# Optimization experiments

Measured on AMD Instinct MI355X. Metric: run time of the kernel, lower is better.

Reference implementation:

```python
import jax, jax.numpy as jnp
import numpy as np

B, S, D = 16, 2048, 128
NEG = -1e9


def setup_inputs() -> dict:
    key = jax.random.key(0)
    kq, kk, kv = jax.random.split(key, 3)
    queries = jax.random.normal(kq, (B, S, D), dtype=jnp.float32)
    keys = jax.random.normal(kk, (B, S, D), dtype=jnp.float32)
    values = jax.random.normal(kv, (B, S, D), dtype=jnp.float32)
    # causal additive mask: 0 on/below diagonal, -1e9 above
    causal = jnp.triu(jnp.ones((S, S), dtype=jnp.float32), k=1) * NEG
    return {"queries": queries, "keys": keys, "values": values, "mask": causal}


def reference(queries, keys, values, mask):
    d = queries.shape[-1]
    scale = 1.0 / jnp.sqrt(jnp.asarray(d, dtype=queries.dtype))
    # scores: [b, q, k]
    scores = jnp.einsum("bqd,bkd->bqk", queries, keys) * scale
    scores = scores + mask  # broadcast [S,S] over batch
    weights = jax.nn.softmax(scores, axis=-1)
    # dropout p=0.0 in eval mode -> identity
    return jnp.einsum("bqk,bkd->bqd", weights, values)
```

## Files before the change

kernel.cpp:

```cpp
#include <hip/hip_runtime.h>
#include <hip/hip_bf16.h>
#include <cstdint>

#define SS   2048
#define DD   128
#define QBLK 64
#define KBLK 64
#define NTILES (SS / KBLK)
#define TILE_BYTES 16384
#define WS_NEED ((size_t)16 * NTILES * TILE_BYTES * 2)

typedef __attribute__((ext_vector_type(8))) short short8;
typedef __attribute__((ext_vector_type(4))) float f32x4;

__device__ __forceinline__ unsigned short f2bf(float x) {
  return __builtin_bit_cast(unsigned short, (__bf16)x);
}

__device__ __forceinline__ int sigma_col(int a) {
  return (a & 35) | ((a & 12) << 1) | ((a & 16) >> 2);
}

__global__ __launch_bounds__(256) void prepack_kv(
    const float* __restrict__ K, const float* __restrict__ V, char* __restrict__ ws)
{
  __shared__ float vf[64][129];
  const int b = blockIdx.x, t = blockIdx.y;
  const int tid = threadIdx.x;
  const float* Kt = K + ((size_t)b * SS + t * KBLK) * DD;
  const float* Vt = V + ((size_t)b * SS + t * KBLK) * DD;
  char* Kd = ws + ((size_t)(b * NTILES + t)) * TILE_BYTES;
  char* Vd = ws + (size_t)16 * NTILES * TILE_BYTES + ((size_t)(b * NTILES + t)) * TILE_BYTES;

  #pragma unroll
  for (int u = 0; u < 4; ++u) {
    int row = u * 16 + (tid >> 4);
    int col = 8 * (tid & 15);
    const float4* sp = reinterpret_cast<const float4*>(Kt + (size_t)row * DD + col);
    float4 x = sp[0], y = sp[1];
    short8 w;
    w[0] = f2bf(x.x); w[1] = f2bf(x.y); w[2] = f2bf(x.z); w[3] = f2bf(x.w);
    w[4] = f2bf(y.x); w[5] = f2bf(y.y); w[6] = f2bf(y.z); w[7] = f2bf(y.w);
    int off = (row * 256 + col * 2) ^ ((row & 7) << 4);
    *reinterpret_cast<short8*>(Kd + off) = w;
  }
  #pragma unroll
  for (int u = 0; u < 4; ++u) {
    int row = u * 16 + (tid >> 4);
    int col = 8 * (tid & 15);
    const float4* sp = reinterpret_cast<const float4*>(Vt + (size_t)row * DD + col);
    float4 x = sp[0], y = sp[1];
    vf[row][col + 0] = x.x; vf[row][col + 1] = x.y; vf[row][col + 2] = x.z; vf[row][col + 3] = x.w;
    vf[row][col + 4] = y.x; vf[row][col + 5] = y.y; vf[row][col + 6] = y.z; vf[row][col + 7] = y.w;
  }
  __syncthreads();
  #pragma unroll
  for (int q = 0; q < 4; ++q) {
    int idx = q * 256 + tid;
    int d = idx >> 3, y = idx & 7;
    short8 w;
    #pragma unroll
    for (int j = 0; j < 8; ++j) {
      int a = (j & 3) | ((y & 3) << 2) | ((j & 4) << 2) | ((y & 4) << 3);
      w[j] = f2bf(vf[a][d]);
    }
    int off = ((d << 7) + (y << 4)) ^ ((((d >> 3) ^ d) & 7) << 4);
    *reinterpret_cast<short8*>(Vd + off) = w;
  }
}

__device__ __forceinline__ void stage_tile(const char* Ksrc, const char* Vsrc,
                                           char* Kl, char* Vl, int wid, int lane)
{
  #pragma unroll
  for (int i = 0; i < 4; ++i) {
    int off = wid * 4096 + i * 1024;
    __builtin_amdgcn_global_load_lds(
        (const __attribute__((address_space(1))) unsigned int*)(Ksrc + off + lane * 16),
        (__attribute__((address_space(3))) unsigned int*)(Kl + off), 16, 0, 0);
  }
  #pragma unroll
  for (int i = 0; i < 4; ++i) {
    int off = wid * 4096 + i * 1024;
    __builtin_amdgcn_global_load_lds(
        (const __attribute__((address_space(1))) unsigned int*)(Vsrc + off + lane * 16),
        (__attribute__((address_space(3))) unsigned int*)(Vl + off), 16, 0, 0);
  }
}

__global__ __launch_bounds__(256) void sdpa_causal_v2(
    const float* __restrict__ Q, const char* __restrict__ ws, float* __restrict__ O)
{
  __shared__ __align__(16) char smem[2 * 32768];

  const int b = blockIdx.x;
  const int y = blockIdx.y;
  const int qb = (y < 16) ? (31 - y) : (y - 16);
  const int q0 = qb * QBLK;
  const int tid = threadIdx.x;
  const int lane = tid & 63;
  const int wid  = tid >> 6;
  const int l15  = lane & 15;
  const int hi   = lane >> 4;

  const float* Qb = Q + (size_t)b * SS * DD;
  float*       Ob = O + (size_t)b * SS * DD;
  const char*  Kws = ws + ((size_t)b * NTILES) * TILE_BYTES;
  const char*  Vws = ws + (size_t)16 * NTILES * TILE_BYTES + ((size_t)b * NTILES) * TILE_BYTES;

  const float scale = 0.08838834764831845f;

  short8 qf[4];
  {
    const float* qrow = Qb + (size_t)(q0 + wid * 16 + l15) * DD;
    #pragma unroll
    for (int c = 0; c < 4; ++c) {
      const float4* p = reinterpret_cast<const float4*>(qrow + 32 * c + 8 * hi);
      float4 x = p[0], y2 = p[1];
      short8 w;
      w[0] = f2bf(x.x * scale); w[1] = f2bf(x.y * scale);
      w[2] = f2bf(x.z * scale); w[3] = f2bf(x.w * scale);
      w[4] = f2bf(y2.x * scale); w[5] = f2bf(y2.y * scale);
      w[6] = f2bf(y2.z * scale); w[7] = f2bf(y2.w * scale);
      qf[c] = w;
    }
  }

  f32x4 o[8];
  #pragma unroll
  for (int nt = 0; nt < 8; ++nt) o[nt] = (f32x4){0.f, 0.f, 0.f, 0.f};
  float m = -INFINITY;
  float lsum = 0.f;

  const int ntile = qb + 1;
  int cur = 0;

  stage_tile(Kws, Vws, smem, smem + 16384, wid, lane);
  __syncthreads();

  for (int t = 0; t < ntile; ++t) {
    if (t + 1 < ntile) {
      char* nb = smem + (cur ^ 1) * 32768;
      stage_tile(Kws + (size_t)(t + 1) * TILE_BYTES, Vws + (size_t)(t + 1) * TILE_BYTES,
                 nb, nb + 16384, wid, lane);
    }

    const char* Kl = smem + cur * 32768;
    const char* Vl = Kl + 16384;
    const int kv0 = t * KBLK;

    f32x4 sacc[4];
    __builtin_amdgcn_s_setprio(1);
    #pragma unroll
    for (int g = 0; g < 4; ++g) {
      f32x4 acc = {0.f, 0.f, 0.f, 0.f};
      #pragma unroll
      for (int c = 0; c < 4; ++c) {
        int row = g * 16 + l15;
        int byteoff = (row * 256 + (32 * c + 8 * hi) * 2) ^ ((row & 7) << 4);
        short8 kf = *reinterpret_cast<const short8*>(Kl + byteoff);
        acc = __builtin_amdgcn_mfma_f32_16x16x32_bf16(kf, qf[c], acc, 0, 0, 0);
      }
      sacc[g] = acc;
    }
    __builtin_amdgcn_s_setprio(0);

    if (t == ntile - 1) {
      const int q = q0 + wid * 16 + l15;
      #pragma unroll
      for (int g = 0; g < 4; ++g)
        #pragma unroll
        for (int i = 0; i < 4; ++i) {
          int key = kv0 + g * 16 + 4 * hi + i;
          if (key > q) sacc[g][i] = -1e30f;
        }
    }

    float tmax = -INFINITY;
    #pragma unroll
    for (int g = 0; g < 4; ++g)
      #pragma unroll
      for (int i = 0; i < 4; ++i) tmax = fmaxf(tmax, sacc[g][i]);
    tmax = fmaxf(tmax, __shfl_xor(tmax, 16));
    tmax = fmaxf(tmax, __shfl_xor(tmax, 32));
    float mnew = fmaxf(m, tmax);
    float corr = __expf(m - mnew);
    m = mnew;

    float p[4][4];
    float psum = 0.f;
    #pragma unroll
    for (int g = 0; g < 4; ++g)
      #pragma unroll
      for (int i = 0; i < 4; ++i) {
        float pv = __expf(sacc[g][i] - mnew);
        p[g][i] = pv;
        psum += pv;
      }
    psum += __shfl_xor(psum, 16);
    psum += __shfl_xor(psum, 32);
    lsum = lsum * corr + psum;

    float corrO[4];
    #pragma unroll
    for (int i = 0; i < 4; ++i) corrO[i] = __shfl(corr, 4 * hi + i);
    #pragma unroll
    for (int nt = 0; nt < 8; ++nt)
      #pragma unroll
      for (int i = 0; i < 4; ++i) o[nt][i] *= corrO[i];

    short8 pf[2];
    #pragma unroll
    for (int ks = 0; ks < 2; ++ks) {
      short8 w;
      #pragma unroll
      for (int i = 0; i < 4; ++i) {
        w[i]     = f2bf(p[2 * ks][i]);
        w[4 + i] = f2bf(p[2 * ks + 1][i]);
      }
      pf[ks] = w;
    }

    __builtin_amdgcn_s_setprio(1);
    #pragma unroll
    for (int ks = 0; ks < 2; ++ks) {
      #pragma unroll
      for (int nt = 0; nt < 8; ++nt) {
        int d = nt * 16 + l15;
        int byteoff = ((d << 7) + (ks * 32 + 8 * hi) * 2) ^ ((((d >> 3) ^ d) & 7) << 4);
        short8 vvf = *reinterpret_cast<const short8*>(Vl + byteoff);
        o[nt] = __builtin_amdgcn_mfma_f32_16x16x32_bf16(pf[ks], vvf, o[nt], 0, 0, 0);
      }
    }
    __builtin_amdgcn_s_setprio(0);

    if (t + 1 < ntile) {
      __syncthreads();
      cur ^= 1;
    }
  }

  float rl = 1.0f / lsum;
  float rlO[4];
  #pragma unroll
  for (int i = 0; i < 4; ++i) rlO[i] = __shfl(rl, 4 * hi + i);
  const int qrow = q0 + wid * 16;
  #pragma unroll
  for (int nt = 0; nt < 8; ++nt)
    #pragma unroll
    for (int i = 0; i < 4; ++i)
      Ob[(size_t)(qrow + 4 * hi + i) * DD + nt * 16 + l15] = o[nt][i] * rlO[i];
}

__global__ __launch_bounds__(256) void sdpa_causal_kernel(
    const float* __restrict__ Q, const float* __restrict__ K,
    const float* __restrict__ V, float* __restrict__ O)
{
  __shared__ __align__(16) char smem[KBLK * DD * 2 + DD * KBLK * 2];
  char* Klds  = smem;
  char* Vtlds = smem + KBLK * DD * 2;

  const int b   = blockIdx.x;
  const int qb  = (int)gridDim.y - 1 - (int)blockIdx.y;
  const int q0  = qb * QBLK;
  const int tid = threadIdx.x;
  const int lane = tid & 63;
  const int wid  = tid >> 6;
  const int l15  = lane & 15;
  const int hi   = lane >> 4;

  const float* Qb = Q + (size_t)b * SS * DD;
  const float* Kb = K + (size_t)b * SS * DD;
  const float* Vb = V + (size_t)b * SS * DD;
  float*       Ob = O + (size_t)b * SS * DD;

  const float scale = 0.08838834764831845f;

  short8 qf[4];
  {
    const float* qrow = Qb + (size_t)(q0 + wid * 16 + l15) * DD;
    #pragma unroll
    for (int c = 0; c < 4; ++c) {
      const float4* p = reinterpret_cast<const float4*>(qrow + 32 * c + 8 * hi);
      float4 x = p[0], y = p[1];
      short8 w;
      w[0] = f2bf(x.x * scale); w[1] = f2bf(x.y * scale);
      w[2] = f2bf(x.z * scale); w[3] = f2bf(x.w * scale);
      w[4] = f2bf(y.x * scale); w[5] = f2bf(y.y * scale);
      w[6] = f2bf(y.z * scale); w[7] = f2bf(y.w * scale);
      qf[c] = w;
    }
  }

  f32x4 o[8];
  #pragma unroll
  for (int nt = 0; nt < 8; ++nt) o[nt] = (f32x4){0.f, 0.f, 0.f, 0.f};
  float m = -INFINITY;
  float lsum = 0.f;

  const int ntile = qb + 1;
  for (int t = 0; t < ntile; ++t) {
    const int kv0 = t * KBLK;
    if (t) __syncthreads();

    #pragma unroll
    for (int u = 0; u < 4; ++u) {
      int row = u * 16 + (tid >> 4);
      int col = 8 * (tid & 15);
      const float4* sp = reinterpret_cast<const float4*>(Kb + (size_t)(kv0 + row) * DD + col);
      float4 x = sp[0], y = sp[1];
      short8 w;
      w[0] = f2bf(x.x); w[1] = f2bf(x.y); w[2] = f2bf(x.z); w[3] = f2bf(x.w);
      w[4] = f2bf(y.x); w[5] = f2bf(y.y); w[6] = f2bf(y.z); w[7] = f2bf(y.w);
      int byteoff = (row * 256 + col * 2) ^ ((row & 7) << 4);
      *reinterpret_cast<short8*>(Klds + byteoff) = w;
    }
    #pragma unroll
    for (int u = 0; u < 4; ++u) {
      int row = u * 16 + (tid >> 4);
      int col = 8 * (tid & 15);
      const float4* sp = reinterpret_cast<const float4*>(Vb + (size_t)(kv0 + row) * DD + col);
      float4 x = sp[0], y = sp[1];
      int sc = sigma_col(row);
      float vals[8] = {x.x, x.y, x.z, x.w, y.x, y.y, y.z, y.w};
      #pragma unroll
      for (int j = 0; j < 8; ++j) {
        int d = col + j;
        int byteoff = ((d << 7) + (sc << 1)) ^ ((((d >> 3) ^ d) & 7) << 4);
        *reinterpret_cast<unsigned short*>(Vtlds + byteoff) = f2bf(vals[j]);
      }
    }
    __syncthreads();

    f32x4 sacc[4];
    #pragma unroll
    for (int g = 0; g < 4; ++g) {
      f32x4 acc = {0.f, 0.f, 0.f, 0.f};
      #pragma unroll
      for (int c = 0; c < 4; ++c) {
        int row = g * 16 + l15;
        int byteoff = (row * 256 + (32 * c + 8 * hi) * 2) ^ ((row & 7) << 4);
        short8 kf = *reinterpret_cast<const short8*>(Klds + byteoff);
        acc = __builtin_amdgcn_mfma_f32_16x16x32_bf16(kf, qf[c], acc, 0, 0, 0);
      }
      sacc[g] = acc;
    }

    if (t == ntile - 1) {
      const int q = q0 + wid * 16 + l15;
      #pragma unroll
      for (int g = 0; g < 4; ++g)
        #pragma unroll
        for (int i = 0; i < 4; ++i) {
          int key = kv0 + g * 16 + 4 * hi + i;
          if (key > q) sacc[g][i] = -1e30f;
        }
    }

    float tmax = -INFINITY;
    #pragma unroll
    for (int g = 0; g < 4; ++g)
      #pragma unroll
      for (int i = 0; i < 4; ++i) tmax = fmaxf(tmax, sacc[g][i]);
    tmax = fmaxf(tmax, __shfl_xor(tmax, 16));
    tmax = fmaxf(tmax, __shfl_xor(tmax, 32));
    float mnew = fmaxf(m, tmax);
    float corr = __expf(m - mnew);
    m = mnew;

    float p[4][4];
    float psum = 0.f;
    #pragma unroll
    for (int g = 0; g < 4; ++g)
      #pragma unroll
      for (int i = 0; i < 4; ++i) {
        float pv = __expf(sacc[g][i] - mnew);
        p[g][i] = pv;
        psum += pv;
      }
    psum += __shfl_xor(psum, 16);
    psum += __shfl_xor(psum, 32);
    lsum = lsum * corr + psum;

    float corrO[4];
    #pragma unroll
    for (int i = 0; i < 4; ++i) corrO[i] = __shfl(corr, 4 * hi + i);
    #pragma unroll
    for (int nt = 0; nt < 8; ++nt)
      #pragma unroll
      for (int i = 0; i < 4; ++i) o[nt][i] *= corrO[i];

    short8 pf[2];
    #pragma unroll
    for (int ks = 0; ks < 2; ++ks) {
      short8 w;
      #pragma unroll
      for (int i = 0; i < 4; ++i) {
        w[i]     = f2bf(p[2 * ks][i]);
        w[4 + i] = f2bf(p[2 * ks + 1][i]);
      }
      pf[ks] = w;
    }

    #pragma unroll
    for (int ks = 0; ks < 2; ++ks) {
      #pragma unroll
      for (int nt = 0; nt < 8; ++nt) {
        int d = nt * 16 + l15;
        int byteoff = ((d << 7) + (ks * 32 + 8 * hi) * 2) ^ ((((d >> 3) ^ d) & 7) << 4);
        short8 vvf = *reinterpret_cast<const short8*>(Vtlds + byteoff);
        o[nt] = __builtin_amdgcn_mfma_f32_16x16x32_bf16(pf[ks], vvf, o[nt], 0, 0, 0);
      }
    }
  }

  float rl = 1.0f / lsum;
  float rlO[4];
  #pragma unroll
  for (int i = 0; i < 4; ++i) rlO[i] = __shfl(rl, 4 * hi + i);
  const int qrow = q0 + wid * 16;
  #pragma unroll
  for (int nt = 0; nt < 8; ++nt)
    #pragma unroll
    for (int i = 0; i < 4; ++i)
      Ob[(size_t)(qrow + 4 * hi + i) * DD + nt * 16 + l15] = o[nt][i] * rlO[i];
}

extern "C" void kernel_launch(void* const* d_in, const int* in_sizes, int n_in,
                              void* d_out, int out_size, void* d_ws, size_t ws_size,
                              hipStream_t stream) {
  const float* Q = (const float*)d_in[0];
  const float* K = (const float*)d_in[1];
  const float* V = (const float*)d_in[2];
  float* O = (float*)d_out;

  if (ws_size >= WS_NEED) {
    char* ws = (char*)d_ws;
    prepack_kv<<<dim3(16, NTILES), 256, 0, stream>>>(K, V, ws);
    sdpa_causal_v2<<<dim3(16, 32), 256, 0, stream>>>(Q, ws, O);
  } else {
    sdpa_causal_kernel<<<dim3(16, 32), 256, 0, stream>>>(Q, K, V, O);
  }
}
```

Before: 64.81 us.

## Split causal attention into balanced KV chunks with partial outputs and merge kernel

The single per-query-block flash kernel is replaced with a split-KV scheme. Each of 640 workgroups handles a 128-row query block against a chunk of up to eight 64-key tiles, chosen by constant lookup tables so the causal work is evenly balanced. A separate merge kernel then sums the bf16 partial outputs and row sums and normalises. The attention inner loop moves to 32x32x16 bf16 MFMAs, folds log2(e) into the query scale, and drops the running-max rescaling in favour of a plain exp2. That removes per-tile max and correction work, but it risks overflow for large scores and adds bf16 rounding of the partials plus an extra kernel launch and workspace traffic.

```diff
diff --git a/kernel.cpp b/kernel.cpp
--- a/kernel.cpp
+++ b/kernel.cpp
@@ -4,24 +4,37 @@
 
 #define SS   2048
 #define DD   128
-#define QBLK 64
 #define KBLK 64
-#define NTILES (SS / KBLK)
+#define NKT  32
 #define TILE_BYTES 16384
-#define WS_NEED ((size_t)16 * NTILES * TILE_BYTES * 2)
-
-typedef __attribute__((ext_vector_type(8))) short short8;
-typedef __attribute__((ext_vector_type(4))) float f32x4;
+#define NBLK 640
+
+#define WS_K   ((size_t)0)
+#define WS_V   ((size_t)16 * NKT * TILE_BYTES)
+#define WS_PO  ((size_t)16 * NKT * TILE_BYTES * 2)
+#define WS_ML  (WS_PO + (size_t)NBLK * 128 * 128 * 2)
+#define WS_NEED (WS_ML + (size_t)NBLK * 128 * 4)
+
+typedef __attribute__((ext_vector_type(8)))  short short8;
+typedef __attribute__((ext_vector_type(16))) float f32x16;
+typedef __attribute__((ext_vector_type(4)))  float f32x4;
 
 __device__ __forceinline__ unsigned short f2bf(float x) {
   return __builtin_bit_cast(unsigned short, (__bf16)x);
 }
-
-__device__ __forceinline__ int sigma_col(int a) {
-  return (a & 35) | ((a & 12) << 1) | ((a & 16) >> 2);
-}
-
-__global__ __launch_bounds__(256) void prepack_kv(
+__device__ __forceinline__ float bfbits2f(unsigned int lo16shifted) {
+  return __builtin_bit_cast(float, lo16shifted);
+}
+
+__device__ __constant__ unsigned char FULLI[28]   = {3,4,5,6,7,7,8,8,9,9,10,10,11,11,11,12,12,12,13,13,13,14,14,14,15,15,15,15};
+__device__ __constant__ unsigned char FULLBASE[16]= {0,0,0,0,1,2,3,4,6,8,10,12,15,18,21,24};
+__device__ __constant__ unsigned char FULLCNT[16] = {0,0,0,1,1,1,1,2,2,2,2,3,3,3,3,4};
+__device__ __constant__ signed   char SMALLIDX[16]= {0,1,2,-1,3,4,5,-1,6,7,8,-1,9,10,11,-1};
+__device__ __constant__ unsigned char SMALLI[12]  = {0,1,2,4,5,6,8,9,10,12,13,14};
+__device__ __constant__ unsigned char SMALLC[12]  = {0,0,0,1,1,1,2,2,2,3,3,3};
+__device__ __constant__ unsigned char SMALLN[12]  = {2,4,6,2,4,6,2,4,6,2,4,6};
+
+__global__ __launch_bounds__(256) void prepack_kv4(
     const float* __restrict__ K, const float* __restrict__ V, char* __restrict__ ws)
 {
   __shared__ float vf[64][129];
@@ -29,8 +42,8 @@
   const int tid = threadIdx.x;
   const float* Kt = K + ((size_t)b * SS + t * KBLK) * DD;
   const float* Vt = V + ((size_t)b * SS + t * KBLK) * DD;
-  char* Kd = ws + ((size_t)(b * NTILES + t)) * TILE_BYTES;
-  char* Vd = ws + (size_t)16 * NTILES * TILE_BYTES + ((size_t)(b * NTILES + t)) * TILE_BYTES;
+  char* Kd = ws + WS_K + ((size_t)(b * NKT + t)) * TILE_BYTES;
+  char* Vd = ws + WS_V + ((size_t)(b * NKT + t)) * TILE_BYTES;
 
   #pragma unroll
   for (int u = 0; u < 4; ++u) {
@@ -50,21 +63,21 @@
     int col = 8 * (tid & 15);
     const float4* sp = reinterpret_cast<const float4*>(Vt + (size_t)row * DD + col);
     float4 x = sp[0], y = sp[1];
-    vf[row][col + 0] = x.x; vf[row][col + 1] = x.y; vf[row][col + 2] = x.z; vf[row][col + 3] = x.w;
-    vf[row][col + 4] = y.x; vf[row][col + 5] = y.y; vf[row][col + 6] = y.z; vf[row][col + 7] = y.w;
+    vf[row][col+0]=x.x; vf[row][col+1]=x.y; vf[row][col+2]=x.z; vf[row][col+3]=x.w;
+    vf[row][col+4]=y.x; vf[row][col+5]=y.y; vf[row][col+6]=y.z; vf[row][col+7]=y.w;
   }
   __syncthreads();
   #pragma unroll
   for (int q = 0; q < 4; ++q) {
     int idx = q * 256 + tid;
-    int d = idx >> 3, y = idx & 7;
+    int d = idx >> 3, y8 = idx & 7;
     short8 w;
     #pragma unroll
     for (int j = 0; j < 8; ++j) {
-      int a = (j & 3) | ((y & 3) << 2) | ((j & 4) << 2) | ((y & 4) << 3);
+      int a = ((y8 >> 2) << 5) | (((y8 >> 1) & 1) << 4) | ((j >> 2) << 3) | (j & 3) | ((y8 & 1) << 2);
       w[j] = f2bf(vf[a][d]);
     }
-    int off = ((d << 7) + (y << 4)) ^ ((((d >> 3) ^ d) & 7) << 4);
+    int off = ((d << 7) + (y8 << 4)) ^ ((d & 7) << 4);
     *reinterpret_cast<short8*>(Vd + off) = w;
   }
 }
@@ -88,15 +101,206 @@
   }
 }
 
-__global__ __launch_bounds__(256) void sdpa_causal_v2(
-    const float* __restrict__ Q, const char* __restrict__ ws, float* __restrict__ O)
+__global__ __launch_bounds__(256, 2) void sdpa_v4(
+    const float* __restrict__ Q, const char* __restrict__ ws,
+    unsigned short* __restrict__ partO, float* __restrict__ partML)
 {
   __shared__ __align__(16) char smem[2 * 32768];
 
-  const int b = blockIdx.x;
-  const int y = blockIdx.y;
-  const int qb = (y < 16) ? (31 - y) : (y - 16);
-  const int q0 = qb * QBLK;
+  const int y = blockIdx.x;
+  int b, i, c, ntile;
+  if (y < 448) { int k = y >> 4; b = y & 15; i = FULLI[k]; c = k - FULLBASE[i]; ntile = 8; }
+  else         { int z = y - 448; int k = z >> 4; b = z & 15; i = SMALLI[k]; c = SMALLC[k]; ntile = SMALLN[k]; }
+
+  const int tid  = threadIdx.x;
+  const int lane = tid & 63;
+  const int wid  = tid >> 6;
+  const int l31  = lane & 31;
+  const int h    = lane >> 5;
+
+  const float* Qb  = Q + (size_t)b * SS * DD;
+  const char*  Kws = ws + WS_K + ((size_t)(b * NKT + 8 * c)) * TILE_BYTES;
+  const char*  Vws = ws + WS_V + ((size_t)(b * NKT + 8 * c)) * TILE_BYTES;
+
+  const float qscale = 0.08838834764831845f * 1.4426950408889634f;
+
+  const int qg = 128 * i + wid * 32 + l31;
+
+  short8 qf[8];
+  {
+    const float* qrow = Qb + (size_t)qg * DD;
+    #pragma unroll
+    for (int s = 0; s < 8; ++s) {
+      const float4* p = reinterpret_cast<const float4*>(qrow + s * 16 + h * 8);
+      float4 x = p[0], z = p[1];
+      short8 w;
+      w[0] = f2bf(x.x * qscale); w[1] = f2bf(x.y * qscale);
+      w[2] = f2bf(x.z * qscale); w[3] = f2bf(x.w * qscale);
+      w[4] = f2bf(z.x * qscale); w[5] = f2bf(z.y * qscale);
+      w[6] = f2bf(z.z * qscale); w[7] = f2bf(z.w * qscale);
+      qf[s] = w;
+    }
+  }
+
+  f32x16 o[4];
+  #pragma unroll
+  for (int dg = 0; dg < 4; ++dg)
+    #pragma unroll
+    for (int r = 0; r < 16; ++r) o[dg][r] = 0.f;
+  float lsum = 0.f;
+
+  int cur = 0;
+  stage_tile(Kws, Vws, smem, smem + 16384, wid, lane);
+  __syncthreads();
+
+  for (int t = 0; t < ntile; ++t) {
+    if (t + 1 < ntile) {
+      char* nb = smem + (cur ^ 1) * 32768;
+      stage_tile(Kws + (size_t)(t + 1) * TILE_BYTES, Vws + (size_t)(t + 1) * TILE_BYTES,
+                 nb, nb + 16384, wid, lane);
+    }
+    const char* Kl = smem + cur * 32768;
+    const char* Vl = Kl + 16384;
+    const bool domask = (8 * c + t) >= 2 * i;
+
+    short8 pf[4];
+    float psum = 0.f;
+
+    #pragma unroll
+    for (int g = 0; g < 2; ++g) {
+      f32x16 acc;
+      #pragma unroll
+      for (int r = 0; r < 16; ++r) acc[r] = 0.f;
+      const int key = g * 32 + l31;
+      const int kbase = key * 256 + h * 16;
+      const int kswz = (key & 7) << 4;
+      __builtin_amdgcn_s_setprio(1);
+      #pragma unroll
+      for (int s = 0; s < 8; ++s) {
+        short8 kf = *reinterpret_cast<const short8*>(Kl + ((kbase + s * 32) ^ kswz));
+        acc = __builtin_amdgcn_mfma_f32_32x32x16_bf16(kf, qf[s], acc, 0, 0, 0);
+      }
+      __builtin_amdgcn_s_setprio(0);
+
+      if (domask) {
+        const int kb = (8 * c + t) * 64 + g * 32 + 4 * h;
+        #pragma unroll
+        for (int r = 0; r < 16; ++r) {
+          int keyg = kb + (r & 3) + 8 * (r >> 2);
+          if (keyg > qg) acc[r] = -1e30f;
+        }
+      }
+
+      float pg[16];
+      #pragma unroll
+      for (int r = 0; r < 16; ++r) pg[r] = exp2f(acc[r]);
+      float s0 = ((pg[0]+pg[1])+(pg[2]+pg[3])) + ((pg[4]+pg[5])+(pg[6]+pg[7]));
+      float s1 = ((pg[8]+pg[9])+(pg[10]+pg[11])) + ((pg[12]+pg[13])+(pg[14]+pg[15]));
+      psum += s0 + s1;
+
+      short8 w0, w1;
+      #pragma unroll
+      for (int j = 0; j < 8; ++j) { w0[j] = f2bf(pg[j]); w1[j] = f2bf(pg[8 + j]); }
+      pf[2 * g]     = w0;
+      pf[2 * g + 1] = w1;
+    }
+    lsum += psum;
+
+    __builtin_amdgcn_s_setprio(1);
+    #pragma unroll
+    for (int dg = 0; dg < 4; ++dg) {
+      const int d = dg * 32 + l31;
+      const int vbase = d * 128 + h * 16;
+      const int vswz = (d & 7) << 4;
+      #pragma unroll
+      for (int s4 = 0; s4 < 4; ++s4) {
+        short8 vf8 = *reinterpret_cast<const short8*>(Vl + ((vbase + s4 * 32) ^ vswz));
+        o[dg] = __builtin_amdgcn_mfma_f32_32x32x16_bf16(vf8, pf[s4], o[dg], 0, 0, 0);
+      }
+    }
+    __builtin_amdgcn_s_setprio(0);
+
+    if (t + 1 < ntile) {
+      __syncthreads();
+      cur ^= 1;
+    }
+  }
+
+  lsum += __shfl_xor(lsum, 32);
+
+  unsigned short* po = partO + (size_t)y * (128 * 128) + (size_t)(wid * 32 + l31) * 128;
+  #pragma unroll
+  for (int dg = 0; dg < 4; ++dg)
+    #pragma unroll
+    for (int rq = 0; rq < 4; ++rq) {
+      int d0 = dg * 32 + 8 * rq + 4 * h;
+      ushort4 u;
+      u.x = f2bf(o[dg][4 * rq + 0]);
+      u.y = f2bf(o[dg][4 * rq + 1]);
+      u.z = f2bf(o[dg][4 * rq + 2]);
+      u.w = f2bf(o[dg][4 * rq + 3]);
+      *reinterpret_cast<ushort4*>(po + d0) = u;
+    }
+  if (h == 0) partML[y * 128 + wid * 32 + l31] = lsum;
+}
+
+__global__ __launch_bounds__(256) void merge_v4(
+    const unsigned short* __restrict__ partO, const float* __restrict__ partML,
+    float* __restrict__ O)
+{
+  const int b = blockIdx.x & 15, i = blockIdx.x >> 4;
+  const int tid = threadIdx.x;
+  const int r = tid >> 1, c0 = (tid & 1) * 64;
+
+  float acc[64];
+  #pragma unroll
+  for (int u = 0; u < 64; ++u) acc[u] = 0.f;
+  float ltot = 0.f;
+
+  const int nf = FULLCNT[i];
+  const int si = SMALLIDX[i];
+  const int nch = nf + (si >= 0 ? 1 : 0);
+
+  for (int c = 0; c < nch; ++c) {
+    int slot = (c < nf) ? ((FULLBASE[i] + c) * 16 + b) : (448 + si * 16 + b);
+    ltot += partML[slot * 128 + r];
+    const uint4* po = reinterpret_cast<const uint4*>(
+        partO + (size_t)slot * (128 * 128) + (size_t)r * 128 + c0);
+    #pragma unroll
+    for (int u = 0; u < 8; ++u) {
+      uint4 v = po[u];
+      acc[u*8+0] += bfbits2f(v.x << 16); acc[u*8+1] += bfbits2f(v.x & 0xffff0000u);
+      acc[u*8+2] += bfbits2f(v.y << 16); acc[u*8+3] += bfbits2f(v.y & 0xffff0000u);
+      acc[u*8+4] += bfbits2f(v.z << 16); acc[u*8+5] += bfbits2f(v.z & 0xffff0000u);
+      acc[u*8+6] += bfbits2f(v.w << 16); acc[u*8+7] += bfbits2f(v.w & 0xffff0000u);
+    }
+  }
+  float inv = 1.0f / ltot;
+  float* orow = O + ((size_t)b * SS + 128 * i + r) * DD + c0;
+  #pragma unroll
+  for (int u = 0; u < 16; ++u) {
+    float4 w;
+    w.x = acc[4*u+0] * inv; w.y = acc[4*u+1] * inv;
+    w.z = acc[4*u+2] * inv; w.w = acc[4*u+3] * inv;
+    reinterpret_cast<float4*>(orow)[u] = w;
+  }
+}
+
+__device__ __forceinline__ int sigma_col(int a) {
+  return (a & 35) | ((a & 12) << 1) | ((a & 16) >> 2);
+}
+
+__global__ __launch_bounds__(256) void sdpa_naive(
+    const float* __restrict__ Q, const float* __restrict__ K,
+    const float* __restrict__ V, float* __restrict__ O)
+{
+  __shared__ __align__(16) char smem[64 * 128 * 2 * 2];
+  char* Klds  = smem;
+  char* Vtlds = smem + 64 * 128 * 2;
+
+  const int b   = blockIdx.x;
+  const int qb  = (int)gridDim.y - 1 - (int)blockIdx.y;
+  const int q0  = qb * 64;
   const int tid = threadIdx.x;
   const int lane = tid & 63;
   const int wid  = tid >> 6;
@@ -104,326 +308,142 @@
   const int hi   = lane >> 4;
 
   const float* Qb = Q + (size_t)b * SS * DD;
+  const float* Kb = K + (size_t)b * SS * DD;
+  const float* Vb = V + (size_t)b * SS * DD;
   float*       Ob = O + (size_t)b * SS * DD;
-  const char*  Kws = ws + ((size_t)b * NTILES) * TILE_BYTES;
-  const char*  Vws = ws + (size_t)16 * NTILES * TILE_BYTES + ((size_t)b * NTILES) * TILE_BYTES;
-
   const float scale = 0.08838834764831845f;
 
   short8 qf[4];
   {
     const float* qrow = Qb + (size_t)(q0 + wid * 16 + l15) * DD;
     #pragma unroll
-    for (int c = 0; c < 4; ++c) {
-      const float4* p = reinterpret_cast<const float4*>(qrow + 32 * c + 8 * hi);
-      float4 x = p[0], y2 = p[1];
+    for (int cc = 0; cc < 4; ++cc) {
+      const float4* p = reinterpret_cast<const float4*>(qrow + 32 * cc + 8 * hi);
+      float4 x = p[0], yv = p[1];
       short8 w;
-      w[0] = f2bf(x.x * scale); w[1] = f2bf(x.y * scale);
-      w[2] = f2bf(x.z * scale); w[3] = f2bf(x.w * scale);
-      w[4] = f2bf(y2.x * scale); w[5] = f2bf(y2.y * scale);
-      w[6] = f2bf(y2.z * scale); w[7] = f2bf(y2.w * scale);
-      qf[c] = w;
+      w[0]=f2bf(x.x*scale); w[1]=f2bf(x.y*scale); w[2]=f2bf(x.z*scale); w[3]=f2bf(x.w*scale);
+      w[4]=f2bf(yv.x*scale); w[5]=f2bf(yv.y*scale); w[6]=f2bf(yv.z*scale); w[7]=f2bf(yv.w*scale);
+      qf[cc] = w;
     }
   }
 
   f32x4 o[8];
   #pragma unroll
-  for (int nt = 0; nt < 8; ++nt) o[nt] = (f32x4){0.f, 0.f, 0.f, 0.f};
-  float m = -INFINITY;
-  float lsum = 0.f;
+  for (int nt = 0; nt < 8; ++nt) o[nt] = (f32x4){0.f,0.f,0.f,0.f};
+  float m = -INFINITY, lsum = 0.f;
 
   const int ntile = qb + 1;
-  int cur = 0;
-
-  stage_tile(Kws, Vws, smem, smem + 16384, wid, lane);
-  __syncthreads();
-
   for (int t = 0; t < ntile; ++t) {
-    if (t + 1 < ntile) {
-      char* nb = smem + (cur ^ 1) * 32768;
-      stage_tile(Kws + (size_t)(t + 1) * TILE_BYTES, Vws + (size_t)(t + 1) * TILE_BYTES,
-                 nb, nb + 16384, wid, lane);
-    }
-
-    const char* Kl = smem + cur * 32768;
-    const char* Vl = Kl + 16384;
-    const int kv0 = t * KBLK;
+    const int kv0 = t * 64;
+    if (t) __syncthreads();
+    #pragma unroll
+    for (int u = 0; u < 4; ++u) {
+      int row = u * 16 + (tid >> 4);
+      int col = 8 * (tid & 15);
+      const float4* sp = reinterpret_cast<const float4*>(Kb + (size_t)(kv0 + row) * DD + col);
+      float4 x = sp[0], yv = sp[1];
+      short8 w;
+      w[0]=f2bf(x.x); w[1]=f2bf(x.y); w[2]=f2bf(x.z); w[3]=f2bf(x.w);
+      w[4]=f2bf(yv.x); w[5]=f2bf(yv.y); w[6]=f2bf(yv.z); w[7]=f2bf(yv.w);
+      int off = (row * 256 + col * 2) ^ ((row & 7) << 4);
+      *reinterpret_cast<short8*>(Klds + off) = w;
+    }
+    #pragma unroll
+    for (int u = 0; u < 4; ++u) {
+      int row = u * 16 + (tid >> 4);
+      int col = 8 * (tid & 15);
+      const float4* sp = reinterpret_cast<const float4*>(Vb + (size_t)(kv0 + row) * DD + col);
+      float4 x = sp[0], yv = sp[1];
+      int sc = sigma_col(row);
+      float vals[8] = {x.x, x.y, x.z, x.w, yv.x, yv.y, yv.z, yv.w};
+      #pragma unroll
+      for (int j = 0; j < 8; ++j) {
+        int d = col + j;
+        int off = ((d << 7) + (sc << 1)) ^ ((((d >> 3) ^ d) & 7) << 4);
+        *reinterpret_cast<unsigned short*>(Vtlds + off) = f2bf(vals[j]);
+      }
+    }
+    __syncthreads();
 
     f32x4 sacc[4];
-    __builtin_amdgcn_s_setprio(1);
     #pragma unroll
     for (int g = 0; g < 4; ++g) {
-      f32x4 acc = {0.f, 0.f, 0.f, 0.f};
-      #pragma unroll
-      for (int c = 0; c < 4; ++c) {
+      f32x4 acc = {0.f,0.f,0.f,0.f};
+      #pragma unroll
+      for (int cc = 0; cc < 4; ++cc) {
         int row = g * 16 + l15;
-        int byteoff = (row * 256 + (32 * c + 8 * hi) * 2) ^ ((row & 7) << 4);
-        short8 kf = *reinterpret_cast<const short8*>(Kl + byteoff);
-        acc = __builtin_amdgcn_mfma_f32_16x16x32_bf16(kf, qf[c], acc, 0, 0, 0);
+        int off = (row * 256 + (32 * cc + 8 * hi) * 2) ^ ((row & 7) << 4);
+        short8 kf = *reinterpret_cast<const short8*>(Klds + off);
+        acc = __builtin_amdgcn_mfma_f32_16x16x32_bf16(kf, qf[cc], acc, 0, 0, 0);
       }
       sacc[g] = acc;
     }
-    __builtin_amdgcn_s_setprio(0);
-
     if (t == ntile - 1) {
       const int q = q0 + wid * 16 + l15;
       #pragma unroll
       for (int g = 0; g < 4; ++g)
         #pragma unroll
-        for (int i = 0; i < 4; ++i) {
-          int key = kv0 + g * 16 + 4 * hi + i;
-          if (key > q) sacc[g][i] = -1e30f;
+        for (int ii = 0; ii < 4; ++ii) {
+          int key = kv0 + g * 16 + 4 * hi + ii;
+          if (key > q) sacc[g][ii] = -1e30f;
         }
     }
-
     float tmax = -INFINITY;
     #pragma unroll
     for (int g = 0; g < 4; ++g)
       #pragma unroll
-      for (int i = 0; i < 4; ++i) tmax = fmaxf(tmax, sacc[g][i]);
+      for (int ii = 0; ii < 4; ++ii) tmax = fmaxf(tmax, sacc[g][ii]);
     tmax = fmaxf(tmax, __shfl_xor(tmax, 16));
     tmax = fmaxf(tmax, __shfl_xor(tmax, 32));
     float mnew = fmaxf(m, tmax);
     float corr = __expf(m - mnew);
     m = mnew;
-
-    float p[4][4];
-    float psum = 0.f;
+    float p[4][4]; float psum = 0.f;
     #pragma unroll
     for (int g = 0; g < 4; ++g)
       #pragma unroll
-      for (int i = 0; i < 4; ++i) {
-        float pv = __expf(sacc[g][i] - mnew);
-        p[g][i] = pv;
-        psum += pv;
+      for (int ii = 0; ii < 4; ++ii) {
+        float pv = __expf(sacc[g][ii] - mnew);
+        p[g][ii] = pv; psum += pv;
       }
     psum += __shfl_xor(psum, 16);
     psum += __shfl_xor(psum, 32);
     lsum = lsum * corr + psum;
-
     float corrO[4];
     #pragma unroll
-    for (int i = 0; i < 4; ++i) corrO[i] = __shfl(corr, 4 * hi + i);
+    for (int ii = 0; ii < 4; ++ii) corrO[ii] = __shfl(corr, 4 * hi + ii);
     #pragma unroll
     for (int nt = 0; nt < 8; ++nt)
       #pragma unroll
-      for (int i = 0; i < 4; ++i) o[nt][i] *= corrO[i];
-
-    short8 pf[2];
+      for (int ii = 0; ii < 4; ++ii) o[nt][ii] *= corrO[ii];
+    short8 pfr[2];
     #pragma unroll
     for (int ks = 0; ks < 2; ++ks) {
       short8 w;
       #pragma unroll
-      for (int i = 0; i < 4; ++i) {
-        w[i]     = f2bf(p[2 * ks][i]);
-        w[4 + i] = f2bf(p[2 * ks + 1][i]);
-      }
-      pf[ks] = w;
-    }
-
-    __builtin_amdgcn_s_setprio(1);
-    #pragma unroll
-    for (int ks = 0; ks < 2; ++ks) {
+      for (int ii = 0; ii < 4; ++ii) { w[ii] = f2bf(p[2*ks][ii]); w[4+ii] = f2bf(p[2*ks+1][ii]); }
+      pfr[ks] = w;
+    }
+    #pragma unroll
+    for (int ks = 0; ks < 2; ++ks)
       #pragma unroll
       for (int nt = 0; nt < 8; ++nt) {
         int d = nt * 16 + l15;
-        int byteoff = ((d << 7) + (ks * 32 + 8 * hi) * 2) ^ ((((d >> 3) ^ d) & 7) << 4);
-        short8 vvf = *reinterpret_cast<const short8*>(Vl + byteoff);
-        o[nt] = __builtin_amdgcn_mfma_f32_16x16x32_bf16(pf[ks], vvf, o[nt], 0, 0, 0);
-      }
-    }
-    __builtin_amdgcn_s_setprio(0);
-
-    if (t + 1 < ntile) {
-      __syncthreads();
-      cur ^= 1;
-    }
-  }
-
+        int off = ((d << 7) + (ks * 32 + 8 * hi) * 2) ^ ((((d >> 3) ^ d) & 7) << 4);
+        short8 vvf = *reinterpret_cast<const short8*>(Vtlds + off);
+        o[nt] = __builtin_amdgcn_mfma_f32_16x16x32_bf16(pfr[ks], vvf, o[nt], 0, 0, 0);
+      }
+  }
   float rl = 1.0f / lsum;
   float rlO[4];
   #pragma unroll
-  for (int i = 0; i < 4; ++i) rlO[i] = __shfl(rl, 4 * hi + i);
+  for (int ii = 0; ii < 4; ++ii) rlO[ii] = __shfl(rl, 4 * hi + ii);
   const int qrow = q0 + wid * 16;
   #pragma unroll
   for (int nt = 0; nt < 8; ++nt)
     #pragma unroll
-    for (int i = 0; i < 4; ++i)
-      Ob[(size_t)(qrow + 4 * hi + i) * DD + nt * 16 + l15] = o[nt][i] * rlO[i];
-}
-
-__global__ __launch_bounds__(256) void sdpa_causal_kernel(
-    const float* __restrict__ Q, const float* __restrict__ K,
-    const float* __restrict__ V, float* __restrict__ O)
-{
-  __shared__ __align__(16) char smem[KBLK * DD * 2 + DD * KBLK * 2];
-  char* Klds  = smem;
-  char* Vtlds = smem + KBLK * DD * 2;
-
-  const int b   = blockIdx.x;
-  const int qb  = (int)gridDim.y - 1 - (int)blockIdx.y;
-  const int q0  = qb * QBLK;
-  const int tid = threadIdx.x;
-  const int lane = tid & 63;
-  const int wid  = tid >> 6;
-  const int l15  = lane & 15;
-  const int hi   = lane >> 4;
-
-  const float* Qb = Q + (size_t)b * SS * DD;
-  const float* Kb = K + (size_t)b * SS * DD;
-  const float* Vb = V + (size_t)b * SS * DD;
-  float*       Ob = O + (size_t)b * SS * DD;
-
-  const float scale = 0.08838834764831845f;
-
-  short8 qf[4];
-  {
-    const float* qrow = Qb + (size_t)(q0 + wid * 16 + l15) * DD;
-    #pragma unroll
-    for (int c = 0; c < 4; ++c) {
-      const float4* p = reinterpret_cast<const float4*>(qrow + 32 * c + 8 * hi);
-      float4 x = p[0], y = p[1];
-      short8 w;
-      w[0] = f2bf(x.x * scale); w[1] = f2bf(x.y * scale);
-      w[2] = f2bf(x.z * scale); w[3] = f2bf(x.w * scale);
-      w[4] = f2bf(y.x * scale); w[5] = f2bf(y.y * scale);
-      w[6] = f2bf(y.z * scale); w[7] = f2bf(y.w * scale);
-      qf[c] = w;
-    }
-  }
-
-  f32x4 o[8];
-  #pragma unroll
-  for (int nt = 0; nt < 8; ++nt) o[nt] = (f32x4){0.f, 0.f, 0.f, 0.f};
-  float m = -INFINITY;
-  float lsum = 0.f;
-
-  const int ntile = qb + 1;
-  for (int t = 0; t < ntile; ++t) {
-    const int kv0 = t * KBLK;
-    if (t) __syncthreads();
-
-    #pragma unroll
-    for (int u = 0; u < 4; ++u) {
-      int row = u * 16 + (tid >> 4);
-      int col = 8 * (tid & 15);
-      const float4* sp = reinterpret_cast<const float4*>(Kb + (size_t)(kv0 + row) * DD + col);
-      float4 x = sp[0], y = sp[1];
-      short8 w;
-      w[0] = f2bf(x.x); w[1] = f2bf(x.y); w[2] = f2bf(x.z); w[3] = f2bf(x.w);
-      w[4] = f2bf(y.x); w[5] = f2bf(y.y); w[6] = f2bf(y.z); w[7] = f2bf(y.w);
-      int byteoff = (row * 256 + col * 2) ^ ((row & 7) << 4);
-      *reinterpret_cast<short8*>(Klds + byteoff) = w;
-    }
-    #pragma unroll
-    for (int u = 0; u < 4; ++u) {
-      int row = u * 16 + (tid >> 4);
-      int col = 8 * (tid & 15);
-      const float4* sp = reinterpret_cast<const float4*>(Vb + (size_t)(kv0 + row) * DD + col);
-      float4 x = sp[0], y = sp[1];
-      int sc = sigma_col(row);
-      float vals[8] = {x.x, x.y, x.z, x.w, y.x, y.y, y.z, y.w};
-      #pragma unroll
-      for (int j = 0; j < 8; ++j) {
-        int d = col + j;
-        int byteoff = ((d << 7) + (sc << 1)) ^ ((((d >> 3) ^ d) & 7) << 4);
-        *reinterpret_cast<unsigned short*>(Vtlds + byteoff) = f2bf(vals[j]);
-      }
-    }
-    __syncthreads();
-
-    f32x4 sacc[4];
-    #pragma unroll
-    for (int g = 0; g < 4; ++g) {
-      f32x4 acc = {0.f, 0.f, 0.f, 0.f};
-      #pragma unroll
-      for (int c = 0; c < 4; ++c) {
-        int row = g * 16 + l15;
-        int byteoff = (row * 256 + (32 * c + 8 * hi) * 2) ^ ((row & 7) << 4);
-        short8 kf = *reinterpret_cast<const short8*>(Klds + byteoff);
-        acc = __builtin_amdgcn_mfma_f32_16x16x32_bf16(kf, qf[c], acc, 0, 0, 0);
-      }
-      sacc[g] = acc;
-    }
-
-    if (t == ntile - 1) {
-      const int q = q0 + wid * 16 + l15;
-      #pragma unroll
-      for (int g = 0; g < 4; ++g)
-        #pragma unroll
-        for (int i = 0; i < 4; ++i) {
-          int key = kv0 + g * 16 + 4 * hi + i;
-          if (key > q) sacc[g][i] = -1e30f;
-        }
-    }
-
-    float tmax = -INFINITY;
-    #pragma unroll
-    for (int g = 0; g < 4; ++g)
-      #pragma unroll
-      for (int i = 0; i < 4; ++i) tmax = fmaxf(tmax, sacc[g][i]);
-    tmax = fmaxf(tmax, __shfl_xor(tmax, 16));
-    tmax = fmaxf(tmax, __shfl_xor(tmax, 32));
-    float mnew = fmaxf(m, tmax);
-    float corr = __expf(m - mnew);
-    m = mnew;
-
-    float p[4][4];
-    float psum = 0.f;
-    #pragma unroll
-    for (int g = 0; g < 4; ++g)
-      #pragma unroll
-      for (int i = 0; i < 4; ++i) {
-        float pv = __expf(sacc[g][i] - mnew);
-        p[g][i] = pv;
-        psum += pv;
-      }
-    psum += __shfl_xor(psum, 16);
-    psum += __shfl_xor(psum, 32);
-    lsum = lsum * corr + psum;
-
-    float corrO[4];
-    #pragma unroll
-    for (int i = 0; i < 4; ++i) corrO[i] = __shfl(corr, 4 * hi + i);
-    #pragma unroll
-    for (int nt = 0; nt < 8; ++nt)
-      #pragma unroll
-      for (int i = 0; i < 4; ++i) o[nt][i] *= corrO[i];
-
-    short8 pf[2];
-    #pragma unroll
-    for (int ks = 0; ks < 2; ++ks) {
-      short8 w;
-      #pragma unroll
-      for (int i = 0; i < 4; ++i) {
-        w[i]     = f2bf(p[2 * ks][i]);
-        w[4 + i] = f2bf(p[2 * ks + 1][i]);
-      }
-      pf[ks] = w;
-    }
-
-    #pragma unroll
-    for (int ks = 0; ks < 2; ++ks) {
-      #pragma unroll
-      for (int nt = 0; nt < 8; ++nt) {
-        int d = nt * 16 + l15;
-        int byteoff = ((d << 7) + (ks * 32 + 8 * hi) * 2) ^ ((((d >> 3) ^ d) & 7) << 4);
-        short8 vvf = *reinterpret_cast<const short8*>(Vtlds + byteoff);
-        o[nt] = __builtin_amdgcn_mfma_f32_16x16x32_bf16(pf[ks], vvf, o[nt], 0, 0, 0);
-      }
-    }
-  }
-
-  float rl = 1.0f / lsum;
-  float rlO[4];
-  #pragma unroll
-  for (int i = 0; i < 4; ++i) rlO[i] = __shfl(rl, 4 * hi + i);
-  const int qrow = q0 + wid * 16;
-  #pragma unroll
-  for (int nt = 0; nt < 8; ++nt)
-    #pragma unroll
-    for (int i = 0; i < 4; ++i)
-      Ob[(size_t)(qrow + 4 * hi + i) * DD + nt * 16 + l15] = o[nt][i] * rlO[i];
+    for (int ii = 0; ii < 4; ++ii)
+      Ob[(size_t)(qrow + 4 * hi + ii) * DD + nt * 16 + l15] = o[nt][ii] * rlO[ii];
 }
 
 extern "C" void kernel_launch(void* const* d_in, const int* in_sizes, int n_in,
@@ -433,12 +453,15 @@
   const float* K = (const float*)d_in[1];
   const float* V = (const float*)d_in[2];
   float* O = (float*)d_out;
+  char* ws = (char*)d_ws;
 
   if (ws_size >= WS_NEED) {
-    char* ws = (char*)d_ws;
-    prepack_kv<<<dim3(16, NTILES), 256, 0, stream>>>(K, V, ws);
-    sdpa_causal_v2<<<dim3(16, 32), 256, 0, stream>>>(Q, ws, O);
+    unsigned short* partO = (unsigned short*)(ws + WS_PO);
+    float* partML = (float*)(ws + WS_ML);
+    prepack_kv4<<<dim3(16, NKT), 256, 0, stream>>>(K, V, ws);
+    sdpa_v4<<<dim3(NBLK), 256, 0, stream>>>(Q, ws, partO, partML);
+    merge_v4<<<dim3(256), 256, 0, stream>>>(partO, partML, O);
   } else {
-    sdpa_causal_kernel<<<dim3(16, 32), 256, 0, stream>>>(Q, K, V, O);
-  }
-}
+    sdpa_naive<<<dim3(16, 32), 256, 0, stream>>>(Q, K, V, O);
+  }
+}
```

Result: no change. 64.46 us (-0.6%).
